# Optimization experiments

Hardware: AMD Instinct MI355X
Metric: run time of the kernel (lower is better)

Reference implementation:

```python
import jax, jax.numpy as jnp
import numpy as np

N_HEADS = 8


def _norm_weights(idx):
    # softmax over where(idx>0, 1, -9e15) along axis 1 -> uniform weights over non-pad slots
    logits = jnp.where(idx > 0, jnp.float32(1.0), jnp.float32(-9e15))
    return jax.nn.softmax(logits, axis=1)


def _layer_norm(x, g, b, eps=1e-6):
    mu = jnp.mean(x, axis=-1, keepdims=True)
    var = jnp.var(x, axis=-1, keepdims=True)
    return (x - mu) * jax.lax.rsqrt(var + eps) * g + b


def _mha_block(x, mask, wq, wk, wv, wo, g, b):
    # standard multi-head self-attention block with residual + layernorm
    B, L, D = x.shape
    hd = D // N_HEADS
    q = (x @ wq).reshape(B, L, N_HEADS, hd)
    k = (x @ wk).reshape(B, L, N_HEADS, hd)
    v = (x @ wv).reshape(B, L, N_HEADS, hd)
    scores = jnp.einsum('bqhd,bkhd->bhqk', q, k) / jnp.float32(np.sqrt(hd))
    scores = jnp.where(mask[:, None, None, :], jnp.float32(-1e9), scores)
    attn = jax.nn.softmax(scores, axis=-1)
    out = jnp.einsum('bhqk,bkhd->bqhd', attn, v).reshape(B, L, D) @ wo
    return _layer_norm(out + x, g, b)


def _forward(data_idx, seq, timestamps, user_level, useq, user_inf, user_cen,
             spread_status, id2vector,
             user_emb, cen_emb, time_emb, pos_emb, inf_emb,
             w1, w2, w3,
             t_wq, t_wk, t_wv, t_wo, t_g, t_b,
             s_wq, s_wk, s_wv, s_wo, s_g, s_b,
             W, W2, f_l1_w, f_l1_b, f_l2_w, f_l2_b, lin_w, lin_b):
    # ---- HGNN layer (hypergraph conv) ----
    tv = w3[0]  # TextVector = weight3[0]
    dot = w3 @ tv
    cos = dot / (jnp.linalg.norm(tv) * jnp.linalg.norm(w3, axis=1))
    inter_nw = jnp.mean(cos)  # scalar

    tweet_hidden = user_emb + cen_emb[user_cen]          # [N, D]
    x = (tweet_hidden @ w1) * inter_nw                   # [N, D]
    nor = _norm_weights(seq)                             # [E, L]
    edge = jnp.einsum('elc,el->ec', x[seq], nor)         # gather + weighted reduce
    edge = jax.nn.relu(edge)
    e1 = edge @ w2                                       # [E, D]
    u_nor = _norm_weights(useq)                          # [N, Lu]
    node = jnp.einsum('nlc,nl->nc', e1[useq], u_nor)     # [N, D]

    # ---- HGSL head ----
    sb = seq[data_idx]                                   # [B, L]
    nor_b = _norm_weights(sb)
    att_mask = sb == 0                                   # PAD == 0
    adj = node[sb]                                       # [B, L, D]

    att_hidden = adj + time_emb[timestamps[data_idx]]
    att_out = _mha_block(att_hidden, att_mask, t_wq, t_wk, t_wv, t_wo, t_g, t_b)
    news = jnp.einsum('blc,bl->bc', att_out, nor_b)
    news = jnp.concatenate([news, spread_status[data_idx][:, 2:] / 3600.0 / 24.0], axis=-1) @ W

    att_hidden_s = adj + inf_emb[user_inf[data_idx]] + pos_emb[user_level[data_idx]]
    att_out_s = _mha_block(att_hidden_s, att_mask, s_wq, s_wk, s_wv, s_wo, s_g, s_b)
    news_s = jnp.einsum('blc,bl->bc', att_out_s, nor_b)
    news_s = jnp.concatenate([news_s, spread_status[data_idx][:, :2]], axis=-1) @ W2

    # Gated fusion (linear3 unused in original forward; id2vector is overwritten/unused)
    emb = jnp.stack([news, news_s], axis=0)              # [2, B, D+2]
    score = jax.nn.softmax(jnp.tanh(emb @ f_l1_w + f_l1_b) @ f_l2_w + f_l2_b, axis=0)
    fused = jnp.sum(score * emb, axis=0)                 # [B, D+2]
    return jax.nn.log_softmax(fused @ lin_w + lin_b, axis=1)


def setup_inputs():
    key = jax.random.key(0)
    ks = jax.random.split(key, 40)
    N, E, L, Lu, D, B, TV = 50000, 10000, 50, 20, 128, 512, 768
    Dw = D + 2
    s = 0.05
    inp = {
        'data_idx': jax.random.randint(ks[0], (B,), 0, E),
        'seq': jax.random.randint(ks[1], (E, L), 0, N),
        'timestamps': jax.random.randint(ks[2], (E, L), 0, 5000),
        'user_level': jax.random.randint(ks[3], (E, L), 0, 50),
        'useq': jax.random.randint(ks[4], (N, Lu), 0, E),
        'user_inf': jax.random.randint(ks[5], (E, L), 0, 200),
        'user_cen': jax.random.randint(ks[6], (N,), 0, 600),
        'spread_status': jax.random.uniform(ks[7], (E, 4), dtype=jnp.float32),
        'id2vector': jax.random.normal(ks[8], (1,), dtype=jnp.float32),
        'user_emb': s * jax.random.normal(ks[9], (N, D), dtype=jnp.float32),
        'cen_emb': s * jax.random.normal(ks[10], (600, D), dtype=jnp.float32),
        'time_emb': s * jax.random.normal(ks[11], (5000, D), dtype=jnp.float32),
        'pos_emb': s * jax.random.normal(ks[12], (50, D), dtype=jnp.float32),
        'inf_emb': s * jax.random.normal(ks[13], (200, D), dtype=jnp.float32),
        'w1': s * jax.random.normal(ks[14], (D, D), dtype=jnp.float32),
        'w2': s * jax.random.normal(ks[15], (D, D), dtype=jnp.float32),
        'w3': s * jax.random.normal(ks[16], (TV, TV), dtype=jnp.float32),
        'W': s * jax.random.normal(ks[17], (Dw, Dw), dtype=jnp.float32),
        'W2': s * jax.random.normal(ks[18], (Dw, Dw), dtype=jnp.float32),
        'f_l1_w': s * jax.random.normal(ks[19], (Dw, Dw), dtype=jnp.float32),
        'f_l1_b': jnp.zeros((Dw,), jnp.float32),
        'f_l2_w': s * jax.random.normal(ks[20], (Dw, 1), dtype=jnp.float32),
        'f_l2_b': jnp.zeros((1,), jnp.float32),
        'lin_w': s * jax.random.normal(ks[21], (Dw, 2), dtype=jnp.float32),
        'lin_b': jnp.zeros((2,), jnp.float32),
    }
    for nm, i in [('t', 22), ('s', 27)]:
        inp[nm + '_wq'] = s * jax.random.normal(ks[i], (D, D), dtype=jnp.float32)
        inp[nm + '_wk'] = s * jax.random.normal(ks[i + 1], (D, D), dtype=jnp.float32)
        inp[nm + '_wv'] = s * jax.random.normal(ks[i + 2], (D, D), dtype=jnp.float32)
        inp[nm + '_wo'] = s * jax.random.normal(ks[i + 3], (D, D), dtype=jnp.float32)
        inp[nm + '_g'] = jnp.ones((D,), jnp.float32)
        inp[nm + '_b'] = jnp.zeros((D,), jnp.float32)
    return inp


def reference(data_idx, seq, timestamps, user_level, useq, user_inf, user_cen,
              spread_status, id2vector,
              user_emb, cen_emb, time_emb, pos_emb, inf_emb,
              w1, w2, w3,
              t_wq, t_wk, t_wv, t_wo, t_g, t_b,
              s_wq, s_wk, s_wv, s_wo, s_g, s_b,
              W, W2, f_l1_w, f_l1_b, f_l2_w, f_l2_b, lin_w, lin_b):
    return _forward(data_idx, seq, timestamps, user_level, useq, user_inf, user_cen,
                    spread_status, id2vector,
                    user_emb, cen_emb, time_emb, pos_emb, inf_emb,
                    w1, w2, w3,
                    t_wq, t_wk, t_wv, t_wo, t_g, t_b,
                    s_wq, s_wk, s_wv, s_wo, s_g, s_b,
                    W, W2, f_l1_w, f_l1_b, f_l2_w, f_l2_b, lin_w, lin_b)
```

## Files before the change

### kernel.cpp

```cpp
#include <hip/hip_runtime.h>
#include <math.h>

constexpr int Nn = 50000;
constexpr int Ee = 10000;
constexpr int Ll = 50;
constexpr int LuU = 20;
constexpr int Dd = 128;
constexpr int Bb = 512;
constexpr int TVv = 768;
constexpr int Dw = 130;
constexpr int BL = Bb * Ll;

typedef __attribute__((ext_vector_type(8))) short bf8v;
typedef __attribute__((ext_vector_type(4))) float f4v;
typedef __attribute__((ext_vector_type(8))) unsigned short u16x8;

__device__ __forceinline__ unsigned short f2bf(float f) {
  union { float f; unsigned u; } v; v.f = f;
  unsigned r = v.u + 0x7FFFu + ((v.u >> 16) & 1u);
  return (unsigned short)(r >> 16);
}
__device__ __forceinline__ float bf2f(unsigned short h) {
  union { unsigned u; float f; } v; v.u = ((unsigned)h) << 16; return v.f;
}
__device__ __forceinline__ int swz(int b) { return b ^ (((b >> 8) & 7) << 4); }

__device__ __forceinline__ float block_sum_256(float v, volatile float* scr) {
#pragma unroll
  for (int o = 32; o > 0; o >>= 1) v += __shfl_down(v, o, 64);
  __syncthreads();
  if ((threadIdx.x & 63) == 0) scr[threadIdx.x >> 6] = v;
  __syncthreads();
  return scr[0] + scr[1] + scr[2] + scr[3];
}

__global__ __launch_bounds__(256) void k_cos(const float* __restrict__ w3,
                                             float* __restrict__ dotb,
                                             float* __restrict__ nrmb) {
  __shared__ float scr[4];
  int i = blockIdx.x;
  const float* row = w3 + (size_t)i * TVv;
  float d = 0.f, n = 0.f;
  for (int j = threadIdx.x; j < TVv; j += 256) {
    float a = row[j];
    d += a * w3[j];
    n += a * a;
  }
  d = block_sum_256(d, scr);
  n = block_sum_256(n, scr);
  if (threadIdx.x == 0) { dotb[i] = d; nrmb[i] = n; }
}

__global__ __launch_bounds__(256) void k_internw(const float* __restrict__ dotb,
                                                 const float* __restrict__ nrmb,
                                                 float* __restrict__ internw) {
  __shared__ float scr[4];
  float n0 = sqrtf(nrmb[0]);
  float s = 0.f;
  for (int i = threadIdx.x; i < TVv; i += 256)
    s += dotb[i] / (n0 * sqrtf(nrmb[i]));
  s = block_sum_256(s, scr);
  if (threadIdx.x == 0) *internw = s / (float)TVv;
}

__global__ __launch_bounds__(256) void k_prep(
    const float* w1, const float* w2,
    const float* twq, const float* twk, const float* twv, const float* two,
    const float* swq, const float* swk, const float* swv, const float* swo,
    unsigned short* __restrict__ out) {
  int wsel = blockIdx.x >> 3, part = blockIdx.x & 7;
  const float* w;
  switch (wsel) {
    case 0: w = w1; break;  case 1: w = w2; break;
    case 2: w = twq; break; case 3: w = twk; break;
    case 4: w = twv; break; case 5: w = two; break;
    case 6: w = swq; break; case 7: w = swk; break;
    case 8: w = swv; break; default: w = swo; break;
  }
  int u = part * 256 + threadIdx.x;
  int n = u >> 4, k0 = (u & 15) * 8;
  u16x8 pv;
#pragma unroll
  for (int i = 0; i < 8; i++) pv[i] = f2bf(w[(size_t)(k0 + i) * Dd + n]);
  ((u16x8*)(out + (size_t)wsel * Dd * Dd))[u] = pv;
}

template <int MODE>
__global__ __launch_bounds__(256) void k_gemm_plain(
    const void* __restrict__ inA, const float* __restrict__ in1,
    const int* __restrict__ gidx, const float* __restrict__ scalep,
    const unsigned short* __restrict__ WTbase,
    const unsigned short* __restrict__ hidT, const unsigned short* __restrict__ hidS,
    unsigned short* __restrict__ outQ, unsigned short* __restrict__ outK,
    unsigned short* __restrict__ outV,
    unsigned short* __restrict__ out0, int nrows) {
  __shared__ unsigned short WT[Dd * Dd];
  __shared__ __align__(16) unsigned short Ab[64 * Dd];

  const unsigned short* Wg;
  const unsigned short* in;
  unsigned short* out;
  int r0;
  if constexpr (MODE == 2) {
    int tile = blockIdx.x % 400, z = blockIdx.x / 400;
    int branch = z / 3, sel = z % 3;
    in = branch ? hidS : hidT;
    Wg = WTbase + (size_t)(2 + branch * 4 + sel) * Dd * Dd;
    unsigned short* o = (sel == 0) ? outQ : (sel == 1) ? outK : outV;
    out = o + (size_t)branch * BL * Dd;
    r0 = tile * 64;
  } else {
    in = (const unsigned short*)inA;
    Wg = WTbase + (size_t)(MODE == 0 ? 0 : 1) * Dd * Dd;
    out = out0;
    r0 = blockIdx.x * 64;
  }

  int tid = threadIdx.x;
  {
    const u16x8* src = (const u16x8*)Wg;
    for (int u = tid; u < 2048; u += 256)
      *(u16x8*)((char*)WT + swz(u * 16)) = src[u];
  }
  if constexpr (MODE == 0) {
    float sc = *scalep;
    for (int u = tid; u < 1024; u += 256) {
      int rr = u >> 4, c0 = (u & 15) * 8;
      int r = r0 + rr;
      u16x8 pv;
      if (r < nrows) {
        const float* a = (const float*)inA + (size_t)r * Dd + c0;
        const float* c = in1 + (size_t)gidx[r] * Dd + c0;
#pragma unroll
        for (int i = 0; i < 8; i++) pv[i] = f2bf((a[i] + c[i]) * sc);
      } else {
#pragma unroll
        for (int i = 0; i < 8; i++) pv[i] = 0;
      }
      *(u16x8*)((char*)Ab + swz(rr * 256 + c0 * 2)) = pv;
    }
  } else {
    for (int u = tid; u < 1024; u += 256) {
      int rr = u >> 4;
      int r = r0 + rr;
      u16x8 pv;
      if (r < nrows) pv = ((const u16x8*)in)[(size_t)r * 16 + (u & 15)];
      else {
#pragma unroll
        for (int i = 0; i < 8; i++) pv[i] = 0;
      }
      *(u16x8*)((char*)Ab + swz(rr * 256 + (u & 15) * 16)) = pv;
    }
  }
  __syncthreads();

  int lane = tid & 63, wid = tid >> 6;
  int lrow = lane & 15, lg = lane >> 4;
  bf8v af[4];
#pragma unroll
  for (int kc = 0; kc < 4; kc++)
    af[kc] = *(const bf8v*)((char*)Ab + swz((wid * 16 + lrow) * 256 + kc * 64 + lg * 16));
  f4v acc[8];
#pragma unroll
  for (int nt = 0; nt < 8; nt++)
#pragma unroll
    for (int j = 0; j < 4; j++) acc[nt][j] = 0.f;
#pragma unroll
  for (int nt = 0; nt < 8; nt++)
#pragma unroll
    for (int kc = 0; kc < 4; kc++) {
      bf8v bfg = *(const bf8v*)((char*)WT + swz((nt * 16 + lrow) * 256 + kc * 64 + lg * 16));
      acc[nt] = __builtin_amdgcn_mfma_f32_16x16x32_bf16(af[kc], bfg, acc[nt], 0, 0, 0);
    }
#pragma unroll
  for (int nt = 0; nt < 8; nt++)
#pragma unroll
    for (int j = 0; j < 4; j++) {
      int r = r0 + wid * 16 + lg * 4 + j;
      if (r < nrows) out[(size_t)r * Dd + nt * 16 + lrow] = f2bf(acc[nt][j]);
    }
}

__global__ __launch_bounds__(256) void k_gemm_ln(
    const unsigned short* __restrict__ ctxall,
    const unsigned short* __restrict__ hidT, const unsigned short* __restrict__ hidS,
    const unsigned short* __restrict__ WTbase,
    const float* __restrict__ tg, const float* __restrict__ tb,
    const float* __restrict__ sg, const float* __restrict__ sb_,
    unsigned short* __restrict__ attall) {
  __shared__ unsigned short WT[Dd * Dd];
  __shared__ __align__(16) char UB[64 * 132 * 4];
  unsigned short* Ab = (unsigned short*)UB;
  float (*O)[132] = (float (*)[132])UB;

  int tile = blockIdx.x % 400, branch = blockIdx.x / 400;
  const unsigned short* in = ctxall + (size_t)branch * BL * Dd;
  const unsigned short* resid = (branch ? hidS : hidT);
  const unsigned short* Wg = WTbase + (size_t)(5 + branch * 4) * Dd * Dd;
  const float* lng = branch ? sg : tg;
  const float* lnb = branch ? sb_ : tb;
  unsigned short* out = attall + (size_t)branch * BL * Dd;
  int r0 = tile * 64;
  int tid = threadIdx.x;

  {
    const u16x8* src = (const u16x8*)Wg;
    for (int u = tid; u < 2048; u += 256)
      *(u16x8*)((char*)WT + swz(u * 16)) = src[u];
  }
  for (int u = tid; u < 1024; u += 256) {
    int rr = u >> 4;
    u16x8 pv = ((const u16x8*)in)[(size_t)(r0 + rr) * 16 + (u & 15)];
    *(u16x8*)((char*)Ab + swz(rr * 256 + (u & 15) * 16)) = pv;
  }
  __syncthreads();

  int lane = tid & 63, wid = tid >> 6;
  int lrow = lane & 15, lg = lane >> 4;
  bf8v af[4];
#pragma unroll
  for (int kc = 0; kc < 4; kc++)
    af[kc] = *(const bf8v*)((char*)Ab + swz((wid * 16 + lrow) * 256 + kc * 64 + lg * 16));
  f4v acc[8];
#pragma unroll
  for (int nt = 0; nt < 8; nt++)
#pragma unroll
    for (int j = 0; j < 4; j++) acc[nt][j] = 0.f;
#pragma unroll
  for (int nt = 0; nt < 8; nt++)
#pragma unroll
    for (int kc = 0; kc < 4; kc++) {
      bf8v bfg = *(const bf8v*)((char*)WT + swz((nt * 16 + lrow) * 256 + kc * 64 + lg * 16));
      acc[nt] = __builtin_amdgcn_mfma_f32_16x16x32_bf16(af[kc], bfg, acc[nt], 0, 0, 0);
    }
  __syncthreads();
#pragma unroll
  for (int nt = 0; nt < 8; nt++)
#pragma unroll
    for (int j = 0; j < 4; j++)
      O[wid * 16 + lg * 4 + j][nt * 16 + lrow] = acc[nt][j];
  __syncthreads();
  int r = tid >> 2, c0 = (tid & 3) * 32;
  size_t gr = (size_t)(r0 + r);
  float vv[32];
  float s1 = 0.f, s2 = 0.f;
#pragma unroll
  for (int i8 = 0; i8 < 4; i8++) {
    u16x8 hb = *(const u16x8*)(resid + gr * Dd + c0 + i8 * 8);
#pragma unroll
    for (int i = 0; i < 8; i++) {
      float x = O[r][c0 + i8 * 8 + i] + bf2f(hb[i]);
      vv[i8 * 8 + i] = x; s1 += x; s2 += x * x;
    }
  }
  s1 += __shfl_xor(s1, 1, 64); s2 += __shfl_xor(s2, 1, 64);
  s1 += __shfl_xor(s1, 2, 64); s2 += __shfl_xor(s2, 2, 64);
  float mu = s1 * (1.f / Dd);
  float var = s2 * (1.f / Dd) - mu * mu;
  float rs = rsqrtf(var + 1e-6f);
#pragma unroll
  for (int i8 = 0; i8 < 4; i8++) {
    u16x8 ov;
#pragma unroll
    for (int i = 0; i < 8; i++) {
      int c = c0 + i8 * 8 + i;
      ov[i] = f2bf((vv[i8 * 8 + i] - mu) * rs * lng[c] + lnb[c]);
    }
    *(u16x8*)(out + gr * Dd + c0 + i8 * 8) = ov;
  }
}

__global__ __launch_bounds__(256) void k_gather_e(const unsigned short* __restrict__ X,
                                                  const int* __restrict__ seq,
                                                  unsigned short* __restrict__ EDGE) {
  int r = blockIdx.x * 16 + (threadIdx.x >> 4);
  int c0 = (threadIdx.x & 15) * 8;
  const int* row = seq + (size_t)r * Ll;
  float acc[8];
#pragma unroll
  for (int i = 0; i < 8; i++) acc[i] = 0.f;
  int cnt = 0;
#pragma unroll 1
  for (int l0 = 0; l0 < Ll; l0 += 10) {
    int ids[10];
#pragma unroll
    for (int t = 0; t < 10; t++) ids[t] = row[l0 + t];
    u16x8 vv[10];
#pragma unroll
    for (int t = 0; t < 10; t++)
      vv[t] = *(const u16x8*)(X + (size_t)ids[t] * Dd + c0);
#pragma unroll
    for (int t = 0; t < 10; t++)
      if (ids[t] > 0) {
        cnt++;
#pragma unroll
        for (int i = 0; i < 8; i++) acc[i] += bf2f(vv[t][i]);
      }
  }
  u16x8 ov;
  if (cnt) {
    float inv = 1.f / (float)cnt;
#pragma unroll
    for (int i = 0; i < 8; i++) ov[i] = f2bf(fmaxf(acc[i] * inv, 0.f));
  } else {
    u16x8 x0 = *(const u16x8*)(X + c0);
#pragma unroll
    for (int i = 0; i < 8; i++) ov[i] = f2bf(fmaxf(bf2f(x0[i]), 0.f));
  }
  *(u16x8*)(EDGE + (size_t)r * Dd + c0) = ov;
}

__global__ __launch_bounds__(256) void k_hidfuse(
    const unsigned short* __restrict__ E1, const int* __restrict__ data_idx,
    const int* __restrict__ seq, const int* __restrict__ tsmp,
    const int* __restrict__ uinf, const int* __restrict__ ulev,
    const int* __restrict__ useq,
    const float* __restrict__ time_emb, const float* __restrict__ inf_emb,
    const float* __restrict__ pos_emb,
    unsigned short* __restrict__ hidTb, unsigned short* __restrict__ hidSb) {
  int bl = blockIdx.x * 16 + (threadIdx.x >> 4);
  int c0 = (threadIdx.x & 15) * 8;
  int b = bl / Ll, l = bl % Ll;
  int e = data_idx[b];
  int sid = seq[(size_t)e * Ll + l];
  const int* urow = useq + (size_t)sid * LuU;
  float acc[8];
#pragma unroll
  for (int i = 0; i < 8; i++) acc[i] = 0.f;
  int cnt = 0;
#pragma unroll 1
  for (int t0 = 0; t0 < LuU; t0 += 10) {
    int ids[10];
#pragma unroll
    for (int t = 0; t < 10; t++) ids[t] = urow[t0 + t];
    u16x8 vv[10];
#pragma unroll
    for (int t = 0; t < 10; t++)
      vv[t] = *(const u16x8*)(E1 + (size_t)ids[t] * Dd + c0);
#pragma unroll
    for (int t = 0; t < 10; t++)
      if (ids[t] > 0) {
        cnt++;
#pragma unroll
        for (int i = 0; i < 8; i++) acc[i] += bf2f(vv[t][i]);
      }
  }
  float node[8];
  if (cnt) {
    float inv = 1.f / (float)cnt;
#pragma unroll
    for (int i = 0; i < 8; i++) node[i] = acc[i] * inv;
  } else {
    u16x8 e0 = *(const u16x8*)(E1 + c0);
#pragma unroll
    for (int i = 0; i < 8; i++) node[i] = bf2f(e0[i]);
  }
  int ts = tsmp[(size_t)e * Ll + l];
  int fi = uinf[(size_t)e * Ll + l];
  int lv = ulev[(size_t)e * Ll + l];
  const float4* tp = (const float4*)(time_emb + (size_t)ts * Dd + c0);
  const float4* ip = (const float4*)(inf_emb + (size_t)fi * Dd + c0);
  const float4* pp = (const float4*)(pos_emb + (size_t)lv * Dd + c0);
  float4 t0 = tp[0], t1 = tp[1];
  float4 i0 = ip[0], i1 = ip[1];
  float4 p0 = pp[0], p1 = pp[1];
  float te[8] = {t0.x, t0.y, t0.z, t0.w, t1.x, t1.y, t1.z, t1.w};
  float ie[8] = {i0.x, i0.y, i0.z, i0.w, i1.x, i1.y, i1.z, i1.w};
  float pe[8] = {p0.x, p0.y, p0.z, p0.w, p1.x, p1.y, p1.z, p1.w};
  u16x8 ht, hs;
#pragma unroll
  for (int i = 0; i < 8; i++) {
    ht[i] = f2bf(node[i] + te[i]);
    hs[i] = f2bf(node[i] + ie[i] + pe[i]);
  }
  size_t o = (size_t)bl * Dd + c0;
  *(u16x8*)(hidTb + o) = ht;
  *(u16x8*)(hidSb + o) = hs;
}

__global__ __launch_bounds__(64) void k_attn(const unsigned short* __restrict__ qall,
                                             const unsigned short* __restrict__ kall,
                                             const unsigned short* __restrict__ vall,
                                             const int* __restrict__ data_idx,
                                             const int* __restrict__ seq,
                                             unsigned short* __restrict__ ctxall) {
  int branch = blockIdx.x >> 12;
  int b = (blockIdx.x >> 3) & 511;
  int h = blockIdx.x & 7;
  size_t boff = (size_t)branch * BL * Dd;
  const unsigned short* q = qall + boff;
  const unsigned short* k = kall + boff;
  const unsigned short* v = vall + boff;
  unsigned short* ctx = ctxall + boff;
  __shared__ float Kl[Ll][16], Vl[Ll][16];
  __shared__ int maskl[Ll];
  int e = data_idx[b];
  for (int i = threadIdx.x; i < Ll; i += 64)
    maskl[i] = (seq[(size_t)e * Ll + i] == 0);
  size_t base = (size_t)b * Ll * Dd + h * 16;
  for (int i = threadIdx.x; i < Ll * 16; i += 64) {
    int l = i >> 4, d = i & 15;
    size_t o = base + (size_t)l * Dd + d;
    Kl[l][d] = bf2f(k[o]);
    Vl[l][d] = bf2f(v[o]);
  }
  __syncthreads();
  int qi = threadIdx.x;
  if (qi < Ll) {
    size_t qo = base + (size_t)qi * Dd;
    const u16x8* qp = (const u16x8*)(q + qo);
    u16x8 q0 = qp[0], q1 = qp[1];
    float qv[16];
#pragma unroll
    for (int d = 0; d < 8; d++) { qv[d] = bf2f(q0[d]); qv[8 + d] = bf2f(q1[d]); }
    float sc[Ll];
    float m = -1e30f;
#pragma unroll
    for (int ki = 0; ki < Ll; ki++) {
      float s;
      if (maskl[ki]) s = -1e9f;
      else {
        s = 0.f;
#pragma unroll
        for (int d = 0; d < 16; d++) s += qv[d] * Kl[ki][d];
        s *= 0.25f;
      }
      sc[ki] = s;
      m = fmaxf(m, s);
    }
    float sum = 0.f;
#pragma unroll
    for (int ki = 0; ki < Ll; ki++) { float p = expf(sc[ki] - m); sc[ki] = p; sum += p; }
    float inv = 1.f / sum;
    float o[16];
#pragma unroll
    for (int d = 0; d < 16; d++) o[d] = 0.f;
#pragma unroll
    for (int ki = 0; ki < Ll; ki++) {
      float p = sc[ki];
#pragma unroll
      for (int d = 0; d < 16; d++) o[d] += p * Vl[ki][d];
    }
    unsigned* cp = (unsigned*)(ctx + qo);
#pragma unroll
    for (int d2 = 0; d2 < 8; d2++) {
      unsigned lo = f2bf(o[2 * d2] * inv), hi = f2bf(o[2 * d2 + 1] * inv);
      cp[d2] = lo | (hi << 16);
    }
  }
}

__global__ __launch_bounds__(128) void k_newsred(const unsigned short* __restrict__ attall,
                                                 const int* __restrict__ data_idx,
                                                 const int* __restrict__ seq,
                                                 const float* __restrict__ spread,
                                                 float* __restrict__ news) {
  __shared__ int sl[Ll];
  __shared__ int scnt;
  int b = blockIdx.x, branch = blockIdx.y;
  int e = data_idx[b];
  const unsigned short* att = attall + (size_t)branch * BL * Dd;
  if (threadIdx.x < Ll) sl[threadIdx.x] = seq[(size_t)e * Ll + threadIdx.x];
  __syncthreads();
  if (threadIdx.x == 0) {
    int c = 0;
    for (int l = 0; l < Ll; l++) c += (sl[l] > 0);
    scnt = c;
  }
  __syncthreads();
  int cnt = scnt;
  float wnp = cnt ? 1.f / (float)cnt : 0.02f;
  int c = threadIdx.x;
  float acc = 0.f;
  for (int l = 0; l < Ll; l++) {
    float w = cnt ? ((sl[l] > 0) ? wnp : 0.f) : wnp;
    acc += w * bf2f(att[((size_t)b * Ll + l) * Dd + c]);
  }
  float* nrow = news + ((size_t)branch * Bb + b) * 132;
  nrow[c] = acc;
  if (c < 2) {
    nrow[Dd + c] = branch ? spread[(size_t)e * 4 + c]
                          : spread[(size_t)e * 4 + 2 + c] * (1.f / 86400.f);
  }
}

__global__ __launch_bounds__(256) void k_newsW(const float* __restrict__ news,
                                               const float* __restrict__ Wm,
                                               const float* __restrict__ W2m,
                                               float* __restrict__ NT,
                                               float* __restrict__ NS) {
  __shared__ float Wl[Dw][Dw + 1];
  __shared__ float nrow[132];
  int branch = blockIdx.y;
  const float* W = branch ? W2m : Wm;
  float* out = branch ? NS : NT;
  for (int u = threadIdx.x; u < Dw * Dw; u += 256)
    Wl[u / Dw][u % Dw] = W[u];
  for (int rr = 0; rr < 32; rr++) {
    int b = blockIdx.x * 32 + rr;
    __syncthreads();
    if (threadIdx.x < Dw)
      nrow[threadIdx.x] = news[((size_t)branch * Bb + b) * 132 + threadIdx.x];
    __syncthreads();
    int j = threadIdx.x;
    if (j < Dw) {
      float acc = 0.f;
      for (int kk = 0; kk < Dw; kk++) acc += nrow[kk] * Wl[kk][j];
      out[(size_t)b * Dw + j] = acc;
    }
  }
}

__global__ __launch_bounds__(256) void k_fusion(const float* __restrict__ nt,
                                                const float* __restrict__ ns,
                                                const float* __restrict__ l1w,
                                                const float* __restrict__ l1b,
                                                const float* __restrict__ l2w,
                                                const float* __restrict__ l2b,
                                                const float* __restrict__ linw,
                                                const float* __restrict__ linb,
                                                float* __restrict__ out) {
  __shared__ float rt[Dw], rs[Dw];
  __shared__ float scr[4];
  int b = blockIdx.x, j = threadIdx.x;
  if (j < Dw) { rt[j] = nt[(size_t)b * Dw + j]; rs[j] = ns[(size_t)b * Dw + j]; }
  __syncthreads();
  float pt = 0.f, ps = 0.f;
  if (j < Dw) {
    float at = l1b[j], as = l1b[j];
    for (int kk = 0; kk < Dw; kk++) {
      float w = l1w[(size_t)kk * Dw + j];
      at += rt[kk] * w;
      as += rs[kk] * w;
    }
    float lw2 = l2w[j];
    pt = tanhf(at) * lw2;
    ps = tanhf(as) * lw2;
  }
  float st = block_sum_256(pt, scr);
  float ss = block_sum_256(ps, scr);
  st += l2b[0]; ss += l2b[0];
  float m = fmaxf(st, ss);
  float e0 = expf(st - m), e1v = expf(ss - m);
  float inv = 1.f / (e0 + e1v);
  float s0 = e0 * inv, s1 = e1v * inv;
  float fj  = (j < Dw) ? (s0 * rt[j] + s1 * rs[j]) : 0.f;
  float w0  = (j < Dw) ? linw[(size_t)j * 2 + 0] : 0.f;
  float w1v = (j < Dw) ? linw[(size_t)j * 2 + 1] : 0.f;
  float l0 = block_sum_256(fj * w0, scr);
  float l1 = block_sum_256(fj * w1v, scr);
  if (j == 0) {
    l0 += linb[0]; l1 += linb[1];
    float mm = fmaxf(l0, l1);
    float lse = mm + logf(expf(l0 - mm) + expf(l1 - mm));
    out[(size_t)b * 2 + 0] = l0 - lse;
    out[(size_t)b * 2 + 1] = l1 - lse;
  }
}

extern "C" void kernel_launch(void* const* d_in, const int* in_sizes, int n_in,
                              void* d_out, int out_size, void* d_ws, size_t ws_size,
                              hipStream_t stream) {
  const int*   data_idx = (const int*)d_in[0];
  const int*   seq      = (const int*)d_in[1];
  const int*   tsmp     = (const int*)d_in[2];
  const int*   ulev     = (const int*)d_in[3];
  const int*   useq     = (const int*)d_in[4];
  const int*   uinf     = (const int*)d_in[5];
  const int*   ucen     = (const int*)d_in[6];
  const float* spread   = (const float*)d_in[7];
  const float* user_emb = (const float*)d_in[9];
  const float* cen_emb  = (const float*)d_in[10];
  const float* time_emb = (const float*)d_in[11];
  const float* pos_emb  = (const float*)d_in[12];
  const float* inf_emb  = (const float*)d_in[13];
  const float* w1       = (const float*)d_in[14];
  const float* w2       = (const float*)d_in[15];
  const float* w3       = (const float*)d_in[16];
  const float* Wm       = (const float*)d_in[17];
  const float* W2m      = (const float*)d_in[18];
  const float* f_l1_w   = (const float*)d_in[19];
  const float* f_l1_b   = (const float*)d_in[20];
  const float* f_l2_w   = (const float*)d_in[21];
  const float* f_l2_b   = (const float*)d_in[22];
  const float* lin_w    = (const float*)d_in[23];
  const float* lin_b    = (const float*)d_in[24];
  const float* t_wq = (const float*)d_in[25];
  const float* t_wk = (const float*)d_in[26];
  const float* t_wv = (const float*)d_in[27];
  const float* t_wo = (const float*)d_in[28];
  const float* t_g  = (const float*)d_in[29];
  const float* t_b  = (const float*)d_in[30];
  const float* s_wq = (const float*)d_in[31];
  const float* s_wk = (const float*)d_in[32];
  const float* s_wv = (const float*)d_in[33];
  const float* s_wo = (const float*)d_in[34];
  const float* s_g  = (const float*)d_in[35];
  const float* s_b  = (const float*)d_in[36];

  char* ws = (char*)d_ws;
  constexpr size_t SZ_WT  = (size_t)10 * Dd * Dd * 2;
  constexpr size_t SZ_XB  = (size_t)Nn * Dd * 2;
  constexpr size_t SZ_EB  = (size_t)Ee * Dd * 2;
  constexpr size_t SZ_BH  = (size_t)BL * Dd * 2;
  constexpr size_t OFF_WT  = 8192;
  constexpr size_t OFF_X   = OFF_WT + SZ_WT;
  constexpr size_t OFF_EDGE= OFF_X + SZ_XB;
  constexpr size_t OFF_E1  = OFF_EDGE + SZ_EB;
  constexpr size_t OFF_HTB = OFF_E1 + SZ_EB;
  constexpr size_t OFF_HSB = OFF_HTB + SZ_BH;
  constexpr size_t OFF_Q   = OFF_HSB + SZ_BH;
  constexpr size_t OFF_K   = OFF_Q + 2 * SZ_BH;
  constexpr size_t OFF_V   = OFF_K + 2 * SZ_BH;
  constexpr size_t OFF_CTX = OFF_V + 2 * SZ_BH;
  constexpr size_t OFF_ATT = OFF_CTX + 2 * SZ_BH;
  constexpr size_t OFF_NEWS= OFF_ATT + 2 * SZ_BH;
  constexpr size_t OFF_NT  = OFF_NEWS + (size_t)2 * Bb * 132 * 4;
  constexpr size_t OFF_NS  = OFF_NT + (size_t)Bb * Dw * 4;

  float* dotb    = (float*)(ws + 0);
  float* nrmb    = (float*)(ws + 3072);
  float* internw = (float*)(ws + 6144);
  unsigned short* WTall = (unsigned short*)(ws + OFF_WT);
  unsigned short* Xb    = (unsigned short*)(ws + OFF_X);
  unsigned short* EDGEb = (unsigned short*)(ws + OFF_EDGE);
  unsigned short* E1b   = (unsigned short*)(ws + OFF_E1);
  unsigned short* HIDTb = (unsigned short*)(ws + OFF_HTB);
  unsigned short* HIDSb = (unsigned short*)(ws + OFF_HSB);
  unsigned short* Qall  = (unsigned short*)(ws + OFF_Q);
  unsigned short* Kall  = (unsigned short*)(ws + OFF_K);
  unsigned short* Vall  = (unsigned short*)(ws + OFF_V);
  unsigned short* CTXall= (unsigned short*)(ws + OFF_CTX);
  unsigned short* ATTall= (unsigned short*)(ws + OFF_ATT);
  float*          NEWS  = (float*)(ws + OFF_NEWS);
  float*          NT    = (float*)(ws + OFF_NT);
  float*          NS    = (float*)(ws + OFF_NS);
  float* outp = (float*)d_out;

  k_prep<<<80, 256, 0, stream>>>(w1, w2, t_wq, t_wk, t_wv, t_wo,
                                 s_wq, s_wk, s_wv, s_wo, WTall);
  k_cos<<<TVv, 256, 0, stream>>>(w3, dotb, nrmb);
  k_internw<<<1, 256, 0, stream>>>(dotb, nrmb, internw);

  k_gemm_plain<0><<<(Nn + 63) / 64, 256, 0, stream>>>(
      user_emb, cen_emb, ucen, internw, WTall,
      nullptr, nullptr, nullptr, nullptr, nullptr, Xb, Nn);
  k_gather_e<<<Ee / 16, 256, 0, stream>>>(Xb, seq, EDGEb);
  k_gemm_plain<1><<<(Ee + 63) / 64, 256, 0, stream>>>(
      EDGEb, nullptr, nullptr, nullptr, WTall,
      nullptr, nullptr, nullptr, nullptr, nullptr, E1b, Ee);
  k_hidfuse<<<BL / 16, 256, 0, stream>>>(E1b, data_idx, seq, tsmp, uinf, ulev, useq,
                                         time_emb, inf_emb, pos_emb, HIDTb, HIDSb);

  k_gemm_plain<2><<<400 * 6, 256, 0, stream>>>(
      nullptr, nullptr, nullptr, nullptr, WTall,
      HIDTb, HIDSb, Qall, Kall, Vall, nullptr, BL);
  k_attn<<<2 * Bb * 8, 64, 0, stream>>>(Qall, Kall, Vall, data_idx, seq, CTXall);
  k_gemm_ln<<<400 * 2, 256, 0, stream>>>(CTXall, HIDTb, HIDSb, WTall,
                                         t_g, t_b, s_g, s_b, ATTall);

  k_newsred<<<dim3(Bb, 2), 128, 0, stream>>>(ATTall, data_idx, seq, spread, NEWS);
  k_newsW<<<dim3(16, 2), 256, 0, stream>>>(NEWS, Wm, W2m, NT, NS);
  k_fusion<<<Bb, 256, 0, stream>>>(NT, NS, f_l1_w, f_l1_b, f_l2_w, f_l2_b,
                                   lin_w, lin_b, outp);

  (void)in_sizes; (void)n_in; (void)out_size; (void)ws_size;
}
```

Before: 369.1 us.

## Use MFMA for attention and fuse the QKV projections into one GEMM kernel

Replaces the scalar per-thread attention kernel with an MFMA version. Each block handles one batch item for one branch, with each wave covering two heads. QK^T and PV run as bf16 MFMAs, and the softmax probabilities are staged through swizzled shared memory. The QKV projection becomes a dedicated kernel that loads a 128-row activation tile once and reuses it against the Q, K and V weights in turn, cutting activation reloads and block count. The trade-offs are more shared memory per block, half the MFMA K-lanes wasted on zero padding for the 16-wide heads, and extra syncs to reload weights between projections.

```diff
diff --git a/kernel.cpp b/kernel.cpp
--- a/kernel.cpp
+++ b/kernel.cpp
@@ -14,6 +14,7 @@
 typedef __attribute__((ext_vector_type(8))) short bf8v;
 typedef __attribute__((ext_vector_type(4))) float f4v;
 typedef __attribute__((ext_vector_type(8))) unsigned short u16x8;
+typedef __attribute__((ext_vector_type(4))) unsigned short u16x4;
 
 __device__ __forceinline__ unsigned short f2bf(float f) {
   union { float f; unsigned u; } v; v.f = f;
@@ -24,6 +25,7 @@
   union { unsigned u; float f; } v; v.u = ((unsigned)h) << 16; return v.f;
 }
 __device__ __forceinline__ int swz(int b) { return b ^ (((b >> 8) & 7) << 4); }
+__device__ __forceinline__ int swzp(int b) { return b ^ (((b >> 7) & 3) << 4); }
 
 __device__ __forceinline__ float block_sum_256(float v, volatile float* scr) {
 #pragma unroll
@@ -89,39 +91,17 @@
 __global__ __launch_bounds__(256) void k_gemm_plain(
     const void* __restrict__ inA, const float* __restrict__ in1,
     const int* __restrict__ gidx, const float* __restrict__ scalep,
-    const unsigned short* __restrict__ WTbase,
-    const unsigned short* __restrict__ hidT, const unsigned short* __restrict__ hidS,
-    unsigned short* __restrict__ outQ, unsigned short* __restrict__ outK,
-    unsigned short* __restrict__ outV,
-    unsigned short* __restrict__ out0, int nrows) {
+    const unsigned short* __restrict__ WTg,
+    unsigned short* __restrict__ out, int nrows) {
   __shared__ unsigned short WT[Dd * Dd];
   __shared__ __align__(16) unsigned short Ab[64 * Dd];
-
-  const unsigned short* Wg;
-  const unsigned short* in;
-  unsigned short* out;
-  int r0;
-  if constexpr (MODE == 2) {
-    int tile = blockIdx.x % 400, z = blockIdx.x / 400;
-    int branch = z / 3, sel = z % 3;
-    in = branch ? hidS : hidT;
-    Wg = WTbase + (size_t)(2 + branch * 4 + sel) * Dd * Dd;
-    unsigned short* o = (sel == 0) ? outQ : (sel == 1) ? outK : outV;
-    out = o + (size_t)branch * BL * Dd;
-    r0 = tile * 64;
-  } else {
-    in = (const unsigned short*)inA;
-    Wg = WTbase + (size_t)(MODE == 0 ? 0 : 1) * Dd * Dd;
-    out = out0;
-    r0 = blockIdx.x * 64;
-  }
-
   int tid = threadIdx.x;
   {
-    const u16x8* src = (const u16x8*)Wg;
+    const u16x8* src = (const u16x8*)WTg;
     for (int u = tid; u < 2048; u += 256)
       *(u16x8*)((char*)WT + swz(u * 16)) = src[u];
   }
+  int r0 = blockIdx.x * 64;
   if constexpr (MODE == 0) {
     float sc = *scalep;
     for (int u = tid; u < 1024; u += 256) {
@@ -144,7 +124,7 @@
       int rr = u >> 4;
       int r = r0 + rr;
       u16x8 pv;
-      if (r < nrows) pv = ((const u16x8*)in)[(size_t)r * 16 + (u & 15)];
+      if (r < nrows) pv = ((const u16x8*)inA)[(size_t)r * 16 + (u & 15)];
       else {
 #pragma unroll
         for (int i = 0; i < 8; i++) pv[i] = 0;
@@ -153,7 +133,6 @@
     }
   }
   __syncthreads();
-
   int lane = tid & 63, wid = tid >> 6;
   int lrow = lane & 15, lg = lane >> 4;
   bf8v af[4];
@@ -179,6 +158,75 @@
       int r = r0 + wid * 16 + lg * 4 + j;
       if (r < nrows) out[(size_t)r * Dd + nt * 16 + lrow] = f2bf(acc[nt][j]);
     }
+}
+
+__global__ __launch_bounds__(256) void k_gemm_qkv(
+    const unsigned short* __restrict__ hidT, const unsigned short* __restrict__ hidS,
+    const unsigned short* __restrict__ WTbase,
+    unsigned short* __restrict__ outQ, unsigned short* __restrict__ outK,
+    unsigned short* __restrict__ outV) {
+  __shared__ unsigned short WT[Dd * Dd];
+  __shared__ __align__(16) unsigned short Ab[128 * Dd];
+  int tile = blockIdx.x % 200, branch = blockIdx.x / 200;
+  const unsigned short* in = branch ? hidS : hidT;
+  int r0 = tile * 128;
+  int tid = threadIdx.x;
+  for (int u = tid; u < 2048; u += 256) {
+    int rr = u >> 4, ch = u & 15;
+    u16x8 pv = ((const u16x8*)in)[(size_t)(r0 + rr) * 16 + ch];
+    *(u16x8*)((char*)Ab + swz(rr * 256 + ch * 16)) = pv;
+  }
+  {
+    const u16x8* srcW = (const u16x8*)(WTbase + (size_t)(2 + branch * 4) * Dd * Dd);
+    for (int u = tid; u < 2048; u += 256)
+      *(u16x8*)((char*)WT + swz(u * 16)) = srcW[u];
+  }
+  __syncthreads();
+  int lane = tid & 63, wid = tid >> 6;
+  int lrow = lane & 15, lg = lane >> 4;
+  bf8v af[2][4];
+#pragma unroll
+  for (int mi = 0; mi < 2; mi++)
+#pragma unroll
+    for (int kc = 0; kc < 4; kc++)
+      af[mi][kc] = *(const bf8v*)((char*)Ab +
+                    swz((wid * 32 + mi * 16 + lrow) * 256 + kc * 64 + lg * 16));
+#pragma unroll 1
+  for (int sel = 0; sel < 3; sel++) {
+    f4v acc[2][8];
+#pragma unroll
+    for (int mi = 0; mi < 2; mi++)
+#pragma unroll
+      for (int nt = 0; nt < 8; nt++)
+#pragma unroll
+        for (int j = 0; j < 4; j++) acc[mi][nt][j] = 0.f;
+#pragma unroll
+    for (int nt = 0; nt < 8; nt++)
+#pragma unroll
+      for (int kc = 0; kc < 4; kc++) {
+        bf8v bfg = *(const bf8v*)((char*)WT + swz((nt * 16 + lrow) * 256 + kc * 64 + lg * 16));
+        acc[0][nt] = __builtin_amdgcn_mfma_f32_16x16x32_bf16(af[0][kc], bfg, acc[0][nt], 0, 0, 0);
+        acc[1][nt] = __builtin_amdgcn_mfma_f32_16x16x32_bf16(af[1][kc], bfg, acc[1][nt], 0, 0, 0);
+      }
+    unsigned short* outb = ((sel == 0) ? outQ : (sel == 1) ? outK : outV)
+                           + (size_t)branch * BL * Dd;
+#pragma unroll
+    for (int mi = 0; mi < 2; mi++)
+#pragma unroll
+      for (int nt = 0; nt < 8; nt++)
+#pragma unroll
+        for (int j = 0; j < 4; j++) {
+          int r = r0 + wid * 32 + mi * 16 + lg * 4 + j;
+          outb[(size_t)r * Dd + nt * 16 + lrow] = f2bf(acc[mi][nt][j]);
+        }
+    if (sel < 2) {
+      __syncthreads();
+      const u16x8* srcW = (const u16x8*)(WTbase + (size_t)(2 + branch * 4 + sel + 1) * Dd * Dd);
+      for (int u = tid; u < 2048; u += 256)
+        *(u16x8*)((char*)WT + swz(u * 16)) = srcW[u];
+      __syncthreads();
+    }
+  }
 }
 
 __global__ __launch_bounds__(256) void k_gemm_ln(
@@ -378,74 +426,146 @@
   *(u16x8*)(hidSb + o) = hs;
 }
 
-__global__ __launch_bounds__(64) void k_attn(const unsigned short* __restrict__ qall,
-                                             const unsigned short* __restrict__ kall,
-                                             const unsigned short* __restrict__ vall,
-                                             const int* __restrict__ data_idx,
-                                             const int* __restrict__ seq,
-                                             unsigned short* __restrict__ ctxall) {
-  int branch = blockIdx.x >> 12;
-  int b = (blockIdx.x >> 3) & 511;
-  int h = blockIdx.x & 7;
-  size_t boff = (size_t)branch * BL * Dd;
-  const unsigned short* q = qall + boff;
-  const unsigned short* k = kall + boff;
-  const unsigned short* v = vall + boff;
+__global__ __launch_bounds__(256) void k_attn_mfma(
+    const unsigned short* __restrict__ qall,
+    const unsigned short* __restrict__ kall,
+    const unsigned short* __restrict__ vall,
+    const int* __restrict__ data_idx,
+    const int* __restrict__ seq,
+    unsigned short* __restrict__ ctxall) {
+  __shared__ __align__(16) unsigned short QKV[3 * 64 * 128];
+  __shared__ __align__(16) unsigned short PT[4 * 64 * 64];
+  __shared__ int maskl[Ll];
+  int b = blockIdx.x, branch = blockIdx.y;
+  size_t boff = (size_t)branch * BL * Dd + (size_t)b * Ll * Dd;
+  const unsigned short* qg = qall + boff;
+  const unsigned short* kg = kall + boff;
+  const unsigned short* vg = vall + boff;
+  int tid = threadIdx.x;
+  int e = data_idx[b];
+  if (tid < Ll) maskl[tid] = (seq[(size_t)e * Ll + tid] == 0);
+  for (int u = tid; u < 3072; u += 256) {
+    int t = u >> 10, rem = u & 1023;
+    int row = rem >> 4, ch = rem & 15;
+    u16x8 pv;
+    if (row < Ll) {
+      const unsigned short* src = (t == 0) ? qg : (t == 1) ? kg : vg;
+      pv = *(const u16x8*)(src + (size_t)row * Dd + ch * 8);
+    } else {
+#pragma unroll
+      for (int i = 0; i < 8; i++) pv[i] = 0;
+    }
+    *(u16x8*)((char*)QKV + t * 16384 + swz(row * 256 + ch * 16)) = pv;
+  }
+  __syncthreads();
+  int lane = tid & 63, wid = tid >> 6;
+  int lrow = lane & 15, lg = lane >> 4;
+  const char* Qb = (const char*)QKV;
+  const char* Kb = (const char*)QKV + 16384;
+  const char* Vb = (const char*)QKV + 32768;
+  char* PTw = (char*)PT + wid * 8192;
   unsigned short* ctx = ctxall + boff;
-  __shared__ float Kl[Ll][16], Vl[Ll][16];
-  __shared__ int maskl[Ll];
-  int e = data_idx[b];
-  for (int i = threadIdx.x; i < Ll; i += 64)
-    maskl[i] = (seq[(size_t)e * Ll + i] == 0);
-  size_t base = (size_t)b * Ll * Dd + h * 16;
-  for (int i = threadIdx.x; i < Ll * 16; i += 64) {
-    int l = i >> 4, d = i & 15;
-    size_t o = base + (size_t)l * Dd + d;
-    Kl[l][d] = bf2f(k[o]);
-    Vl[l][d] = bf2f(v[o]);
-  }
-  __syncthreads();
-  int qi = threadIdx.x;
-  if (qi < Ll) {
-    size_t qo = base + (size_t)qi * Dd;
-    const u16x8* qp = (const u16x8*)(q + qo);
-    u16x8 q0 = qp[0], q1 = qp[1];
-    float qv[16];
-#pragma unroll
-    for (int d = 0; d < 8; d++) { qv[d] = bf2f(q0[d]); qv[8 + d] = bf2f(q1[d]); }
-    float sc[Ll];
-    float m = -1e30f;
-#pragma unroll
-    for (int ki = 0; ki < Ll; ki++) {
-      float s;
-      if (maskl[ki]) s = -1e9f;
-      else {
-        s = 0.f;
-#pragma unroll
-        for (int d = 0; d < 16; d++) s += qv[d] * Kl[ki][d];
-        s *= 0.25f;
-      }
-      sc[ki] = s;
-      m = fmaxf(m, s);
-    }
-    float sum = 0.f;
-#pragma unroll
-    for (int ki = 0; ki < Ll; ki++) { float p = expf(sc[ki] - m); sc[ki] = p; sum += p; }
-    float inv = 1.f / sum;
-    float o[16];
-#pragma unroll
-    for (int d = 0; d < 16; d++) o[d] = 0.f;
-#pragma unroll
-    for (int ki = 0; ki < Ll; ki++) {
-      float p = sc[ki];
-#pragma unroll
-      for (int d = 0; d < 16; d++) o[d] += p * Vl[ki][d];
-    }
-    unsigned* cp = (unsigned*)(ctx + qo);
-#pragma unroll
-    for (int d2 = 0; d2 < 8; d2++) {
-      unsigned lo = f2bf(o[2 * d2] * inv), hi = f2bf(o[2 * d2 + 1] * inv);
-      cp[d2] = lo | (hi << 16);
+
+#pragma unroll 1
+  for (int hi = 0; hi < 2; hi++) {
+    int h = wid * 2 + hi;
+    int cb = h * 32;
+    bf8v af[4], bf[4];
+    if (lg < 2) {
+#pragma unroll
+      for (int mt = 0; mt < 4; mt++)
+        af[mt] = *(const bf8v*)(Kb + swz((mt * 16 + lrow) * 256 + cb + lg * 16));
+#pragma unroll
+      for (int nt = 0; nt < 4; nt++)
+        bf[nt] = *(const bf8v*)(Qb + swz((nt * 16 + lrow) * 256 + cb + lg * 16));
+    } else {
+#pragma unroll
+      for (int t = 0; t < 4; t++)
+#pragma unroll
+        for (int i = 0; i < 8; i++) { af[t][i] = 0; bf[t][i] = 0; }
+    }
+    f4v acc[16];
+#pragma unroll
+    for (int t = 0; t < 16; t++)
+#pragma unroll
+      for (int j = 0; j < 4; j++) acc[t][j] = 0.f;
+#pragma unroll
+    for (int mt = 0; mt < 4; mt++)
+#pragma unroll
+      for (int nt = 0; nt < 4; nt++)
+        acc[mt * 4 + nt] =
+            __builtin_amdgcn_mfma_f32_16x16x32_bf16(af[mt], bf[nt], acc[mt * 4 + nt], 0, 0, 0);
+#pragma unroll
+    for (int mt = 0; mt < 4; mt++)
+#pragma unroll
+      for (int j = 0; j < 4; j++) {
+        int kk = mt * 16 + lg * 4 + j;
+        bool pad = (kk >= Ll);
+        bool mk = !pad && (maskl[pad ? 0 : kk] != 0);
+#pragma unroll
+        for (int nt = 0; nt < 4; nt++) {
+          float v = acc[mt * 4 + nt][j] * 0.25f;
+          v = mk ? -1e9f : v;
+          v = pad ? -3.0e38f : v;
+          acc[mt * 4 + nt][j] = v;
+        }
+      }
+#pragma unroll
+    for (int nt = 0; nt < 4; nt++) {
+      float m = -3.0e38f;
+#pragma unroll
+      for (int mt = 0; mt < 4; mt++)
+#pragma unroll
+        for (int j = 0; j < 4; j++) m = fmaxf(m, acc[mt * 4 + nt][j]);
+      m = fmaxf(m, __shfl_xor(m, 16, 64));
+      m = fmaxf(m, __shfl_xor(m, 32, 64));
+      float s = 0.f;
+#pragma unroll
+      for (int mt = 0; mt < 4; mt++)
+#pragma unroll
+        for (int j = 0; j < 4; j++) {
+          float p = expf(acc[mt * 4 + nt][j] - m);
+          acc[mt * 4 + nt][j] = p;
+          s += p;
+        }
+      s += __shfl_xor(s, 16, 64);
+      s += __shfl_xor(s, 32, 64);
+      float inv = 1.f / s;
+      int q = nt * 16 + lrow;
+#pragma unroll
+      for (int mt = 0; mt < 4; mt++) {
+        u16x4 pw;
+#pragma unroll
+        for (int j = 0; j < 4; j++) pw[j] = f2bf(acc[mt * 4 + nt][j] * inv);
+        *(u16x4*)(PTw + swzp(q * 128 + mt * 32 + lg * 8)) = pw;
+      }
+    }
+    f4v pacc[4];
+#pragma unroll
+    for (int nt = 0; nt < 4; nt++)
+#pragma unroll
+      for (int j = 0; j < 4; j++) pacc[nt][j] = 0.f;
+#pragma unroll
+    for (int kt = 0; kt < 2; kt++) {
+      bf8v av;
+#pragma unroll
+      for (int i = 0; i < 8; i++)
+        av[i] = *(const short*)(Vb + swz((kt * 32 + lg * 8 + i) * 256 + cb + lrow * 2));
+#pragma unroll
+      for (int nt = 0; nt < 4; nt++) {
+        bf8v bv = *(const bf8v*)(PTw + swzp((nt * 16 + lrow) * 128 + kt * 64 + lg * 16));
+        pacc[nt] = __builtin_amdgcn_mfma_f32_16x16x32_bf16(av, bv, pacc[nt], 0, 0, 0);
+      }
+    }
+#pragma unroll
+    for (int nt = 0; nt < 4; nt++) {
+      int q = nt * 16 + lrow;
+      if (q < Ll) {
+        u16x4 ow;
+#pragma unroll
+        for (int j = 0; j < 4; j++) ow[j] = f2bf(pacc[nt][j]);
+        *(u16x4*)(ctx + (size_t)q * Dd + h * 16 + lg * 4) = ow;
+      }
     }
   }
 }
@@ -643,19 +763,15 @@
   k_internw<<<1, 256, 0, stream>>>(dotb, nrmb, internw);
 
   k_gemm_plain<0><<<(Nn + 63) / 64, 256, 0, stream>>>(
-      user_emb, cen_emb, ucen, internw, WTall,
-      nullptr, nullptr, nullptr, nullptr, nullptr, Xb, Nn);
+      user_emb, cen_emb, ucen, internw, WTall + 0 * Dd * Dd, Xb, Nn);
   k_gather_e<<<Ee / 16, 256, 0, stream>>>(Xb, seq, EDGEb);
   k_gemm_plain<1><<<(Ee + 63) / 64, 256, 0, stream>>>(
-      EDGEb, nullptr, nullptr, nullptr, WTall,
-      nullptr, nullptr, nullptr, nullptr, nullptr, E1b, Ee);
+      EDGEb, nullptr, nullptr, nullptr, WTall + 1 * Dd * Dd, E1b, Ee);
   k_hidfuse<<<BL / 16, 256, 0, stream>>>(E1b, data_idx, seq, tsmp, uinf, ulev, useq,
                                          time_emb, inf_emb, pos_emb, HIDTb, HIDSb);
 
-  k_gemm_plain<2><<<400 * 6, 256, 0, stream>>>(
-      nullptr, nullptr, nullptr, nullptr, WTall,
-      HIDTb, HIDSb, Qall, Kall, Vall, nullptr, BL);
-  k_attn<<<2 * Bb * 8, 64, 0, stream>>>(Qall, Kall, Vall, data_idx, seq, CTXall);
+  k_gemm_qkv<<<400, 256, 0, stream>>>(HIDTb, HIDSb, WTall, Qall, Kall, Vall);
+  k_attn_mfma<<<dim3(Bb, 2), 256, 0, stream>>>(Qall, Kall, Vall, data_idx, seq, CTXall);
   k_gemm_ln<<<400 * 2, 256, 0, stream>>>(CTXall, HIDTb, HIDSb, WTall,
                                          t_g, t_b, s_g, s_b, ATTall);
 
```

New measurement: 357.9 us. 1.03x faster.
